# Kernel optimization log

Measured on AMD Instinct MI355X. Metric: run time of the kernel, lower is better.

## Reference

```python
import jax, jax.numpy as jnp
import numpy as np

B, S, D = 64, 512, 256
HG = 128   # graph-RNN hidden
HE = 128   # edge-RNN hidden (must equal HG: graph state seeds edge layer-0 hidden)
M = 64     # edge lookback window / edge-RNN input size


def _rnn_layer(x, Wih, Whh, bih, bhh):
    # tanh-RNN layer, batch_first. x: [B,S,Din] -> [B,S,H]
    def step(h, xt):
        h = jnp.tanh(xt @ Wih.T + bih + h @ Whh.T + bhh)
        return h, h
    h0 = jnp.zeros((x.shape[0], Whh.shape[0]), x.dtype)
    _, ys = jax.lax.scan(step, h0, jnp.swapaxes(x, 0, 1))
    return jnp.swapaxes(ys, 0, 1)


def _forward(x, mask,
             g_Wih0, g_Whh0, g_bih0, g_bhh0,
             g_Wih1, g_Whh1, g_bih1, g_bhh1,
             e_Wih0, e_Whh0, e_bih0, e_bhh0,
             e_Wih1, e_Whh1, e_bih1, e_bhh1,
             cls_W, cls_b):
    # --- node-level (graph) RNN, 2 layers; padded steps zeroed (pad_packed behavior)
    Y = _rnn_layer(x, g_Wih0, g_Whh0, g_bih0, g_bhh0)
    Y = _rnn_layer(Y, g_Wih1, g_Whh1, g_bih1, g_bhh1)
    Y = Y * mask[..., None].astype(Y.dtype)            # [B,S,HG]

    N = B * S
    gs = Y.reshape(N, HG)                              # graph state seeds layer-0 hidden
    node_i = jnp.tile(jnp.arange(S), B)                # position within sequence
    m = jnp.minimum(node_i, M)                         # steps per node = min(i, M)
    A0 = jnp.zeros((N, M), Y.dtype)

    def estep(carry, j):
        A, h0, h1 = carry
        n0 = jnp.tanh(A @ e_Wih0.T + e_bih0 + h0 @ e_Whh0.T + e_bhh0)
        n1 = jnp.tanh(n0 @ e_Wih1.T + e_bih1 + h1 @ e_Whh1.T + e_bhh1)
        s = jax.nn.sigmoid(n1 @ cls_W.T + cls_b)[:, 0]
        A = A.at[:, j].set(jnp.where(j < m, s, jnp.zeros_like(s)))
        return (A, n0, n1), None

    (A, _, _), _ = jax.lax.scan(estep, (A0, gs, jnp.zeros_like(gs)), jnp.arange(M))
    A = A.reshape(B, S, M)

    # --- banded adjacency: row i gets A[i, :min(i,M)] at cols [max(0,i-M), i), then transpose
    i = jnp.arange(S)
    cols = jnp.maximum(0, i - M)[:, None] + jnp.arange(M)[None, :]   # [S,M]
    valid = jnp.arange(M)[None, :] < jnp.minimum(i, M)[:, None]
    cols = jnp.where(valid, cols, S)                                 # OOB -> dropped
    adj = jnp.zeros((B, S, S), Y.dtype).at[:, i[:, None], cols].set(
        A * valid.astype(A.dtype), mode="drop")
    adj = jnp.swapaxes(adj, 1, 2)
    return Y, adj


def setup_inputs() -> dict:
    key = jax.random.key(0)
    ks = jax.random.split(key, 20)
    sc = jnp.float32(0.1)
    p = lambda k, shp: sc * jax.random.normal(k, shp, jnp.float32)
    return {
        "x": jax.random.normal(ks[0], (B, S, D), jnp.float32),
        "mask": jnp.ones((B, S), jnp.int32),
        "g_Wih0": p(ks[1], (HG, D)), "g_Whh0": p(ks[2], (HG, HG)),
        "g_bih0": p(ks[3], (HG,)), "g_bhh0": p(ks[4], (HG,)),
        "g_Wih1": p(ks[5], (HG, HG)), "g_Whh1": p(ks[6], (HG, HG)),
        "g_bih1": p(ks[7], (HG,)), "g_bhh1": p(ks[8], (HG,)),
        "e_Wih0": p(ks[9], (HE, M)), "e_Whh0": p(ks[10], (HE, HE)),
        "e_bih0": p(ks[11], (HE,)), "e_bhh0": p(ks[12], (HE,)),
        "e_Wih1": p(ks[13], (HE, HE)), "e_Whh1": p(ks[14], (HE, HE)),
        "e_bih1": p(ks[15], (HE,)), "e_bhh1": p(ks[16], (HE,)),
        "cls_W": p(ks[17], (1, HE)), "cls_b": p(ks[18], (1,)),
    }


def reference(x, mask,
              g_Wih0, g_Whh0, g_bih0, g_bhh0,
              g_Wih1, g_Whh1, g_bih1, g_bhh1,
              e_Wih0, e_Whh0, e_bih0, e_bhh0,
              e_Wih1, e_Whh1, e_bih1, e_bhh1,
              cls_W, cls_b):
    return _forward(x, mask,
                    g_Wih0, g_Whh0, g_bih0, g_bhh0,
                    g_Wih1, g_Whh1, g_bih1, g_bhh1,
                    e_Wih0, e_Whh0, e_bih0, e_bhh0,
                    e_Wih1, e_Whh1, e_bih1, e_bhh1,
                    cls_W, cls_b)
```

## Files before the change

### kernel.cpp

```cpp
#include <hip/hip_runtime.h>

#define B_ 64
#define S_ 512
#define D_ 256
#define H_ 128
#define M_ 64
#define N_ (B_ * S_)
#define YSZ ((size_t)N_ * H_)
#define ADJSZ ((size_t)B_ * S_ * S_)

typedef __attribute__((ext_vector_type(8))) _Float16 f16x8;
typedef __attribute__((ext_vector_type(2))) _Float16 h2;
typedef __attribute__((ext_vector_type(4))) float f32x4;

#define MFMAH(a, b, c) __builtin_amdgcn_mfma_f32_16x16x32_f16(a, b, c, 0, 0, 0)

#define BARL() asm volatile("s_waitcnt lgkmcnt(0)\n\ts_barrier" ::: "memory")

#if __has_builtin(__builtin_amdgcn_fdot2)
#define FDOT2(a, b, c) __builtin_amdgcn_fdot2((a), (b), (c), false)
#else
__device__ __forceinline__ float FDOT2(h2 a, h2 b, float c) {
  return c + (float)a.x * (float)b.x + (float)a.y * (float)b.y;
}
#endif

#define WFRAGS (8 * 14)
#define WBYTES ((size_t)WFRAGS * 64 * 16)

__device__ __forceinline__ float fast_tanh(float x) {
  float e = __builtin_amdgcn_exp2f(x * 2.8853900817779268f);
  float r = __builtin_amdgcn_rcpf(e + 1.0f);
  return fmaf(-2.0f, r, 1.0f);
}
__device__ __forceinline__ float fast_sigmoid(float x) {
  float e = __builtin_amdgcn_exp2f(x * -1.4426950408889634f);
  return __builtin_amdgcn_rcpf(1.0f + e);
}

__device__ __forceinline__ int sw(int row, int col, int Kc) {
  return row * Kc + ((((col >> 3) ^ (row & 7)) << 3) | (col & 7));
}
__device__ __forceinline__ int swu(int row, int g) {
  return row * 128 + (((g ^ (row & 7)) << 3));
}

__device__ __forceinline__ f16x8 pack8(float4 a, float4 b) {
  f16x8 r;
  r[0] = (_Float16)a.x; r[1] = (_Float16)a.y;
  r[2] = (_Float16)a.z; r[3] = (_Float16)a.w;
  r[4] = (_Float16)b.x; r[5] = (_Float16)b.y;
  r[6] = (_Float16)b.z; r[7] = (_Float16)b.w;
  return r;
}

__global__ __launch_bounds__(256) void k0_prep(
    const float* __restrict__ eWih0, const float* __restrict__ eWhh0,
    const float* __restrict__ eWih1, const float* __restrict__ eWhh1,
    unsigned short* __restrict__ Wf) {
  int t = blockIdx.x * 256 + threadIdx.x;
  if (t >= WFRAGS * 64) return;
  int fid = t >> 6, lane = t & 63;
  int ntg = fid / 14, kc = fid % 14;
  int j = ntg * 16 + (lane & 15);
  int kbase = (kc < 6 ? kc : kc - 6) * 32 + (lane >> 4) * 8;
  unsigned pk[4];
#pragma unroll
  for (int ii = 0; ii < 4; ++ii) {
    unsigned p2 = 0;
#pragma unroll
    for (int s = 0; s < 2; ++s) {
      int k = kbase + ii * 2 + s;
      float wv;
      if (kc < 6)
        wv = (k < 64) ? eWih0[j * 64 + k] : eWhh0[j * 128 + (k - 64)];
      else
        wv = (k < 128) ? eWih1[j * 128 + k] : eWhh1[j * 128 + (k - 128)];
      _Float16 h = (_Float16)wv;
      unsigned short us = *(unsigned short*)&h;
      p2 |= ((unsigned)us) << (16 * s);
    }
    pk[ii] = p2;
  }
  ((uint4*)Wf)[fid * 64 + lane] = make_uint4(pk[0], pk[1], pk[2], pk[3]);
}

__global__ __launch_bounds__(256) void k1_gemm(
    const float* __restrict__ x, const float* __restrict__ W,
    const float* __restrict__ bih, const float* __restrict__ bhh,
    float* __restrict__ P0) {
  __shared__ float Xs[32][132];
  __shared__ float Ws[32][132];
  const int t = threadIdx.x;
  const int ty = t >> 4, tx = t & 15;
  const int n0 = blockIdx.x * 128;
  float acc[8][8];
#pragma unroll
  for (int i = 0; i < 8; ++i)
#pragma unroll
    for (int j = 0; j < 8; ++j) acc[i][j] = 0.f;

  for (int kc = 0; kc < 256; kc += 32) {
    __syncthreads();
#pragma unroll
    for (int l = 0; l < 4; ++l) {
      int idx = t + l * 256;
      int r = idx >> 3, f4 = idx & 7;
      float4 v = *(const float4*)&x[(size_t)(n0 + r) * 256 + kc + f4 * 4];
      Xs[f4 * 4 + 0][r] = v.x; Xs[f4 * 4 + 1][r] = v.y;
      Xs[f4 * 4 + 2][r] = v.z; Xs[f4 * 4 + 3][r] = v.w;
      float4 wv = *(const float4*)&W[(size_t)r * 256 + kc + f4 * 4];
      Ws[f4 * 4 + 0][r] = wv.x; Ws[f4 * 4 + 1][r] = wv.y;
      Ws[f4 * 4 + 2][r] = wv.z; Ws[f4 * 4 + 3][r] = wv.w;
    }
    __syncthreads();
#pragma unroll
    for (int kk = 0; kk < 32; ++kk) {
      float4 xa = *(const float4*)&Xs[kk][ty * 8];
      float4 xb = *(const float4*)&Xs[kk][ty * 8 + 4];
      float4 wa = *(const float4*)&Ws[kk][tx * 8];
      float4 wb = *(const float4*)&Ws[kk][tx * 8 + 4];
      float xr[8] = {xa.x, xa.y, xa.z, xa.w, xb.x, xb.y, xb.z, xb.w};
      float wr[8] = {wa.x, wa.y, wa.z, wa.w, wb.x, wb.y, wb.z, wb.w};
#pragma unroll
      for (int i = 0; i < 8; ++i)
#pragma unroll
        for (int j = 0; j < 8; ++j) acc[i][j] += xr[i] * wr[j];
    }
  }
  float bias[8];
#pragma unroll
  for (int j = 0; j < 8; ++j) bias[j] = bih[tx * 8 + j] + bhh[tx * 8 + j];
#pragma unroll
  for (int i = 0; i < 8; ++i) {
    float4 s0 = make_float4(acc[i][0] + bias[0], acc[i][1] + bias[1],
                            acc[i][2] + bias[2], acc[i][3] + bias[3]);
    float4 s1 = make_float4(acc[i][4] + bias[4], acc[i][5] + bias[5],
                            acc[i][6] + bias[6], acc[i][7] + bias[7]);
    size_t base = (size_t)(n0 + ty * 8 + i) * 128 + tx * 8;
    *(float4*)&P0[base] = s0;
    *(float4*)&P0[base + 4] = s1;
  }
}

#define K2STEP(S, PP)                                                         \
  {                                                                           \
    if (isL0 && (S) < 512) {                                                  \
      const int rd0 = ((S)&1) ^ 1;                                            \
      f32x4 acc[2];                                                           \
      _Pragma("unroll") for (int i = 0; i < 2; ++i)                           \
          acc[i] = __builtin_bit_cast(f32x4, PP[i]);                          \
      _Pragma("unroll") for (int kc = 0; kc < 4; ++kc) {                      \
        f16x8 bf = *(const f16x8*)&h0s[rd0][swu(colB, kc * 4 + q)];           \
        _Pragma("unroll") for (int i = 0; i < 2; ++i)                         \
            acc[i] = MFMAH(WA[i][kc], bf, acc[i]);                            \
      }                                                                       \
      int tn = ((S) + 2 < 512) ? (S) + 2 : 511;                               \
      _Pragma("unroll") for (int i = 0; i < 2; ++i)                           \
          PP[i] = *(const float4*)(p0base[i] + (size_t)tn * 128);             \
      _Pragma("unroll") for (int i = 0; i < 2; ++i) {                         \
        float v0 = fast_tanh(acc[i][0]), v1 = fast_tanh(acc[i][1]);           \
        float v2 = fast_tanh(acc[i][2]), v3 = fast_tanh(acc[i][3]);           \
        int nb = (wl * 2 + i) * 16 + q * 4;                                   \
        int g = nb >> 3;                                                      \
        int idx = colB * 128 + (((g ^ (colB & 7)) << 3) | (nb & 7));          \
        h2 lo = {(_Float16)v0, (_Float16)v1};                                 \
        h2 hi = {(_Float16)v2, (_Float16)v3};                                 \
        uint2 u = {__builtin_bit_cast(unsigned, lo),                          \
                   __builtin_bit_cast(unsigned, hi)};                         \
        *(uint2*)&h0s[(S)&1][idx] = u;                                        \
      }                                                                       \
    } else if (!isL0 && (S) >= 1) {                                           \
      const int t = (S)-1;                                                    \
      const int rb = t & 1;                                                   \
      f32x4 acc[2], accB[2];                                                  \
      _Pragma("unroll") for (int i = 0; i < 2; ++i) {                         \
        acc[i] = b1v[i];                                                      \
        accB[i] = (f32x4){0.f, 0.f, 0.f, 0.f};                                \
      }                                                                       \
      _Pragma("unroll") for (int kc = 0; kc < 4; ++kc) {                      \
        f16x8 bf = *(const f16x8*)&h0s[rb][swu(colB, kc * 4 + q)];            \
        if ((kc & 1) == 0) {                                                  \
          _Pragma("unroll") for (int i = 0; i < 2; ++i)                       \
              acc[i] = MFMAH(WA[i][kc], bf, acc[i]);                          \
        } else {                                                              \
          _Pragma("unroll") for (int i = 0; i < 2; ++i)                       \
              accB[i] = MFMAH(WA[i][kc], bf, accB[i]);                        \
        }                                                                     \
      }                                                                       \
      _Pragma("unroll") for (int kc = 0; kc < 4; ++kc) {                      \
        f16x8 bf = *(const f16x8*)&h1s[rb ^ 1][swu(colB, kc * 4 + q)];        \
        if ((kc & 1) == 0) {                                                  \
          _Pragma("unroll") for (int i = 0; i < 2; ++i)                       \
              acc[i] = MFMAH(WB[i][kc], bf, acc[i]);                          \
        } else {                                                              \
          _Pragma("unroll") for (int i = 0; i < 2; ++i)                       \
              accB[i] = MFMAH(WB[i][kc], bf, accB[i]);                        \
        }                                                                     \
      }                                                                       \
      float m = mk[colB][t];                                                  \
      _Pragma("unroll") for (int i = 0; i < 2; ++i) {                         \
        f32x4 at = acc[i] + accB[i];                                          \
        float v0 = fast_tanh(at[0]), v1 = fast_tanh(at[1]);                   \
        float v2 = fast_tanh(at[2]), v3 = fast_tanh(at[3]);                   \
        int nb = (wl * 2 + i) * 16 + q * 4;                                   \
        int g = nb >> 3;                                                      \
        int idx = colB * 128 + (((g ^ (colB & 7)) << 3) | (nb & 7));          \
        h2 lo = {(_Float16)v0, (_Float16)v1};                                 \
        h2 hi = {(_Float16)v2, (_Float16)v3};                                 \
        uint2 u = {__builtin_bit_cast(unsigned, lo),                          \
                   __builtin_bit_cast(unsigned, hi)};                         \
        *(uint2*)&h1s[rb][idx] = u;                                           \
        float4 yv = {v0 * m, v1 * m, v2 * m, v3 * m};                         \
        *(float4*)&Y[((size_t)(b0 + colB) * 512 + t) * 128 + nb] = yv;        \
      }                                                                       \
    }                                                                         \
    BARL();                                                                   \
  }

__global__ __launch_bounds__(512, 1) void k2_v10(
    const float* __restrict__ P0, const float* __restrict__ Whh0,
    const float* __restrict__ Wih1, const float* __restrict__ Whh1,
    const float* __restrict__ bih1, const float* __restrict__ bhh1,
    const int* __restrict__ mask, float* __restrict__ Y) {
  __shared__ _Float16 h0s[2][16 * 128];
  __shared__ _Float16 h1s[2][16 * 128];
  __shared__ float mk[16][516];
  const int tid = threadIdx.x;
  const int w = tid >> 6, l = tid & 63;
  const int b0 = blockIdx.x * 16;
  const int colB = l & 15;
  const int q = l >> 4;
  const bool isL0 = (w < 4);
  const int wl = isL0 ? w : (w - 4);

  for (int i = tid; i < 16 * 512; i += 512) {
    int bb = i >> 9, t = i & 511;
    mk[bb][t] = (float)mask[(b0 + bb) * 512 + t];
  }
  for (int i = tid; i < 1024; i += 512) {
    ((unsigned*)&h0s[1][0])[i] = 0u;
    ((unsigned*)&h1s[1][0])[i] = 0u;
  }

  f16x8 WA[2][4];
  f16x8 WB[2][4];
  {
    const float* src = isL0 ? Whh0 : Wih1;
#pragma unroll
    for (int i = 0; i < 2; ++i)
#pragma unroll
      for (int kc = 0; kc < 4; ++kc) {
        const float* r =
            src + ((wl * 2 + i) * 16 + colB) * 128 + kc * 32 + q * 8;
        WA[i][kc] = pack8(*(const float4*)r, *(const float4*)(r + 4));
      }
    if (!isL0) {
#pragma unroll
      for (int i = 0; i < 2; ++i)
#pragma unroll
        for (int kc = 0; kc < 4; ++kc) {
          const float* r =
              Whh1 + ((wl * 2 + i) * 16 + colB) * 128 + kc * 32 + q * 8;
          WB[i][kc] = pack8(*(const float4*)r, *(const float4*)(r + 4));
        }
    }
  }
  f32x4 b1v[2];
  const float* p0base[2];
#pragma unroll
  for (int i = 0; i < 2; ++i) {
    int nb = (wl * 2 + i) * 16 + q * 4;
    if (!isL0) {
      b1v[i] = (f32x4){bih1[nb] + bhh1[nb], bih1[nb + 1] + bhh1[nb + 1],
                       bih1[nb + 2] + bhh1[nb + 2], bih1[nb + 3] + bhh1[nb + 3]};
    } else {
      b1v[i] = (f32x4){0.f, 0.f, 0.f, 0.f};
    }
    p0base[i] = P0 + (size_t)(b0 + colB) * 512 * 128 + nb;
  }
  float4 pp0[2], pp1[2];
  if (isL0) {
#pragma unroll
    for (int i = 0; i < 2; ++i) {
      pp0[i] = *(const float4*)(p0base[i]);
      pp1[i] = *(const float4*)(p0base[i] + 128);
    }
  }
  __syncthreads();

  for (int s2 = 0; s2 < 512; s2 += 2) {
    K2STEP(s2, pp0);
    K2STEP(s2 + 1, pp1);
  }
  K2STEP(512, pp0);
}

#define K3_A(g) ((_Float16*)(sm + (g) * 8192))
#define K3_R(g, i) ((_Float16*)(sm + 16384 + ((g) * 3 + (i)) * 16384))
#define K3_PS(g) ((float*)(sm + 114688 + (g) * 1024))
#define LDSTOT 116736

__global__ __launch_bounds__(512, 2) void k3_edge_f16(
    const float* __restrict__ Y, const unsigned short* __restrict__ Wf,
    const float* __restrict__ bih0, const float* __restrict__ bhh0,
    const float* __restrict__ bih1, const float* __restrict__ bhh1,
    const float* __restrict__ clsW, const float* __restrict__ clsb,
    float* __restrict__ adj) {
  extern __shared__ char sm[];
  const int tid = threadIdx.x;
  const int w = tid >> 6, l = tid & 63;
  const int mg = w & 1, ng = w >> 1;
  const int colL = l & 15, q = l >> 4;
  const int node0 = blockIdx.x * 128;

  for (int i = tid; i < 4096; i += 512) ((unsigned*)sm)[i] = 0u;
  for (int i = tid; i < 4096; i += 512) {
    ((unsigned*)K3_R(0, 2))[i] = 0u;
    ((unsigned*)K3_R(1, 2))[i] = 0u;
  }
  for (int i = tid; i < 16384; i += 512) {
    int nn = i >> 7, k = i & 127;
    float v = Y[(size_t)(node0 + nn) * 128 + k];
    K3_R(nn >> 6, 0)[sw(nn & 63, k, 128)] = (_Float16)v;
  }

  f16x8 Wr[2][14];
#pragma unroll
  for (int nt = 0; nt < 2; ++nt)
#pragma unroll
    for (int kc = 0; kc < 14; ++kc)
      Wr[nt][kc] =
          ((const f16x8*)Wf)[(size_t)(((2 * ng + nt) * 14) + kc) * 64 + l];

  f32x4 b0v[2], b1v[2];
  h2 cw2[2][2];
#pragma unroll
  for (int nt = 0; nt < 2; ++nt) {
    int f0 = (2 * ng + nt) * 16 + q * 4;
    b0v[nt] = (f32x4){bih0[f0] + bhh0[f0], bih0[f0 + 1] + bhh0[f0 + 1],
                      bih0[f0 + 2] + bhh0[f0 + 2], bih0[f0 + 3] + bhh0[f0 + 3]};
    b1v[nt] = (f32x4){bih1[f0] + bhh1[f0], bih1[f0 + 1] + bhh1[f0 + 1],
                      bih1[f0 + 2] + bhh1[f0 + 2], bih1[f0 + 3] + bhh1[f0 + 3]};
    cw2[nt][0].x = (_Float16)clsW[f0];
    cw2[nt][0].y = (_Float16)clsW[f0 + 1];
    cw2[nt][1].x = (_Float16)clsW[f0 + 2];
    cw2[nt][1].y = (_Float16)clsW[f0 + 3];
  }
  const float cbias = clsb[0];
  int mval[2];
  mval[0] = min(((node0 + 0) & 511) + l, 64);
  mval[1] = min(((node0 + 64) & 511) + l, 64);

  int woff[2][2];
#pragma unroll
  for (int mt = 0; mt < 2; ++mt)
#pragma unroll
    for (int nt = 0; nt < 2; ++nt) {
      int node = mg * 32 + mt * 16 + colL;
      int f0 = (2 * ng + nt) * 16 + q * 4;
      woff[mt][nt] =
          node * 128 + ((((f0 >> 3) ^ (node & 7)) << 3) | (f0 & 7));
    }

  __syncthreads();

  int ba = 0, bbv = 1, bc = 2;
  for (int step = 0; step < 64; ++step) {
    _Float16* p_n0rd[2] = {K3_R(0, ba), K3_R(1, ba)};
    _Float16* p_n0wr[2] = {K3_R(0, bbv), K3_R(1, bbv)};
    _Float16* p_n1rd[2] = {K3_R(0, bc), K3_R(1, bc)};
    _Float16* p_n1wr[2] = {K3_R(0, ba), K3_R(1, ba)};

    f32x4 acc[2][2][2];
    f32x4 acc2[2][2][2];
#pragma unroll
    for (int g = 0; g < 2; ++g)
#pragma unroll
      for (int mt = 0; mt < 2; ++mt)
#pragma unroll
        for (int nt = 0; nt < 2; ++nt) {
          acc[g][mt][nt] = b0v[nt];
          acc2[g][mt][nt] = b1v[nt];
        }
#pragma unroll
    for (int kc = 0; kc < 4; ++kc) {
      int gk = kc * 4 + q;
      f16x8 bh[2][2];
#pragma unroll
      for (int g = 0; g < 2; ++g)
#pragma unroll
        for (int mt = 0; mt < 2; ++mt) {
          int row = mg * 32 + mt * 16 + colL;
          bh[g][mt] =
              *(const f16x8*)&p_n0rd[g][row * 128 + ((gk ^ (row & 7)) << 3)];
        }
#pragma unroll
      for (int g = 0; g < 2; ++g)
#pragma unroll
        for (int mt = 0; mt < 2; ++mt)
#pragma unroll
          for (int nt = 0; nt < 2; ++nt)
            acc[g][mt][nt] = MFMAH(Wr[nt][2 + kc], bh[g][mt], acc[g][mt][nt]);
    }
#pragma unroll
    for (int kc = 4; kc < 8; ++kc) {
      int gk = (kc & 3) * 4 + q;
      f16x8 bh[2][2];
#pragma unroll
      for (int g = 0; g < 2; ++g)
#pragma unroll
        for (int mt = 0; mt < 2; ++mt) {
          int row = mg * 32 + mt * 16 + colL;
          bh[g][mt] =
              *(const f16x8*)&p_n1rd[g][row * 128 + ((gk ^ (row & 7)) << 3)];
        }
#pragma unroll
      for (int g = 0; g < 2; ++g)
#pragma unroll
        for (int mt = 0; mt < 2; ++mt)
#pragma unroll
          for (int nt = 0; nt < 2; ++nt)
            acc2[g][mt][nt] =
                MFMAH(Wr[nt][6 + kc], bh[g][mt], acc2[g][mt][nt]);
    }
    if (step > 0) {
      {
        int gk = q;
        f16x8 bh[2][2];
#pragma unroll
        for (int g = 0; g < 2; ++g)
#pragma unroll
          for (int mt = 0; mt < 2; ++mt) {
            int row = mg * 32 + mt * 16 + colL;
            bh[g][mt] =
                *(const f16x8*)&K3_A(g)[row * 64 + ((gk ^ (row & 7)) << 3)];
          }
#pragma unroll
        for (int g = 0; g < 2; ++g)
#pragma unroll
          for (int mt = 0; mt < 2; ++mt)
#pragma unroll
            for (int nt = 0; nt < 2; ++nt)
              acc[g][mt][nt] = MFMAH(Wr[nt][0], bh[g][mt], acc[g][mt][nt]);
      }
      if (step > 32) {
        int gk = 4 + q;
        f16x8 bh[2][2];
#pragma unroll
        for (int g = 0; g < 2; ++g)
#pragma unroll
          for (int mt = 0; mt < 2; ++mt) {
            int row = mg * 32 + mt * 16 + colL;
            bh[g][mt] =
                *(const f16x8*)&K3_A(g)[row * 64 + ((gk ^ (row & 7)) << 3)];
          }
#pragma unroll
        for (int g = 0; g < 2; ++g)
#pragma unroll
          for (int mt = 0; mt < 2; ++mt)
#pragma unroll
            for (int nt = 0; nt < 2; ++nt)
              acc[g][mt][nt] = MFMAH(Wr[nt][1], bh[g][mt], acc[g][mt][nt]);
      }
    }
#pragma unroll
    for (int g = 0; g < 2; ++g)
#pragma unroll
      for (int mt = 0; mt < 2; ++mt)
#pragma unroll
        for (int nt = 0; nt < 2; ++nt) {
          float t0 = fast_tanh(acc[g][mt][nt][0]);
          float t1 = fast_tanh(acc[g][mt][nt][1]);
          float t2 = fast_tanh(acc[g][mt][nt][2]);
          float t3 = fast_tanh(acc[g][mt][nt][3]);
          h2 lo = {(_Float16)t0, (_Float16)t1};
          h2 hi = {(_Float16)t2, (_Float16)t3};
          uint2 u = {__builtin_bit_cast(unsigned, lo),
                     __builtin_bit_cast(unsigned, hi)};
          *(uint2*)&p_n0wr[g][woff[mt][nt]] = u;
        }
    __syncthreads();

#pragma unroll
    for (int kc = 0; kc < 4; ++kc) {
      int gk = kc * 4 + q;
      f16x8 bh[2][2];
#pragma unroll
      for (int g = 0; g < 2; ++g)
#pragma unroll
        for (int mt = 0; mt < 2; ++mt) {
          int row = mg * 32 + mt * 16 + colL;
          bh[g][mt] =
              *(const f16x8*)&p_n0wr[g][row * 128 + ((gk ^ (row & 7)) << 3)];
        }
#pragma unroll
      for (int g = 0; g < 2; ++g)
#pragma unroll
        for (int mt = 0; mt < 2; ++mt)
#pragma unroll
          for (int nt = 0; nt < 2; ++nt)
            acc2[g][mt][nt] =
                MFMAH(Wr[nt][6 + kc], bh[g][mt], acc2[g][mt][nt]);
    }
    float paf[2][2];
#pragma unroll
    for (int g = 0; g < 2; ++g)
#pragma unroll
      for (int mt = 0; mt < 2; ++mt) paf[g][mt] = 0.f;
#pragma unroll
    for (int g = 0; g < 2; ++g)
#pragma unroll
      for (int mt = 0; mt < 2; ++mt)
#pragma unroll
        for (int nt = 0; nt < 2; ++nt) {
          float t0 = fast_tanh(acc2[g][mt][nt][0]);
          float t1 = fast_tanh(acc2[g][mt][nt][1]);
          float t2 = fast_tanh(acc2[g][mt][nt][2]);
          float t3 = fast_tanh(acc2[g][mt][nt][3]);
          h2 lo = {(_Float16)t0, (_Float16)t1};
          h2 hi = {(_Float16)t2, (_Float16)t3};
          paf[g][mt] = FDOT2(cw2[nt][0], lo, paf[g][mt]);
          paf[g][mt] = FDOT2(cw2[nt][1], hi, paf[g][mt]);
          uint2 u = {__builtin_bit_cast(unsigned, lo),
                     __builtin_bit_cast(unsigned, hi)};
          *(uint2*)&p_n1wr[g][woff[mt][nt]] = u;
        }
#pragma unroll
    for (int g = 0; g < 2; ++g)
#pragma unroll
      for (int mt = 0; mt < 2; ++mt) {
        float s = paf[g][mt];
        s += __shfl_xor(s, 16);
        s += __shfl_xor(s, 32);
        paf[g][mt] = s;
      }
    if (q == 0) {
#pragma unroll
      for (int g = 0; g < 2; ++g)
#pragma unroll
        for (int mt = 0; mt < 2; ++mt)
          K3_PS(g)[ng * 64 + mg * 32 + mt * 16 + colL] = paf[g][mt];
    }
    __syncthreads();

    {
      float* ps0 = K3_PS(0);
      float* ps1 = K3_PS(1);
      float s0 = cbias + ps0[l] + ps0[64 + l] + ps0[128 + l] + ps0[192 + l];
      float s1 = cbias + ps1[l] + ps1[64 + l] + ps1[128 + l] + ps1[192 + l];
      float sg0 = fast_sigmoid(s0);
      float sg1 = fast_sigmoid(s1);
      int aidx = l * 64 + ((((step >> 3) ^ (l & 7)) << 3) | (step & 7));
      if (step < mval[0]) K3_A(0)[aidx] = (_Float16)sg0;
      if (step < mval[1]) K3_A(1)[aidx] = (_Float16)sg1;
    }
    int tmp = ba; ba = bbv; bbv = bc; bc = tmp;
  }
  __syncthreads();

#pragma unroll
  for (int g = 0; g < 2; ++g) {
    const int qd = l & 15;
    const int rg4 = l >> 4;
    const int node0g = node0 + g * 64;
    const int ii0 = node0g & 511;
    const int badj = node0g >> 9;
    _Float16* Ag = K3_A(g);
    for (int rb = 0; rb < 64; rb += 4) {
      int r = w * 64 + rb + rg4;
      float4 v;
      float* vp = (float*)&v;
#pragma unroll
      for (int c = 0; c < 4; ++c) {
        int n = qd * 4 + c;
        int ii = ii0 + n;
        int base = (ii - 64 > 0) ? ii - 64 : 0;
        int mv = min(ii, 64);
        int k = r - base;
        float val = 0.f;
        if (k >= 0 && k < mv) val = (float)Ag[sw(n, k, 64)];
        vp[c] = val;
      }
      *(float4*)&adj[((size_t)badj * 512 + r) * 512 + ii0 + qd * 4] = v;
    }
  }
}

extern "C" void kernel_launch(void* const* d_in, const int* in_sizes, int n_in,
                              void* d_out, int out_size, void* d_ws,
                              size_t ws_size, hipStream_t stream) {
  const float* x = (const float*)d_in[0];
  const int* mask = (const int*)d_in[1];
  const float* gWih0 = (const float*)d_in[2];
  const float* gWhh0 = (const float*)d_in[3];
  const float* gbih0 = (const float*)d_in[4];
  const float* gbhh0 = (const float*)d_in[5];
  const float* gWih1 = (const float*)d_in[6];
  const float* gWhh1 = (const float*)d_in[7];
  const float* gbih1 = (const float*)d_in[8];
  const float* gbhh1 = (const float*)d_in[9];
  const float* eWih0 = (const float*)d_in[10];
  const float* eWhh0 = (const float*)d_in[11];
  const float* ebih0 = (const float*)d_in[12];
  const float* ebhh0 = (const float*)d_in[13];
  const float* eWih1 = (const float*)d_in[14];
  const float* eWhh1 = (const float*)d_in[15];
  const float* ebih1 = (const float*)d_in[16];
  const float* ebhh1 = (const float*)d_in[17];
  const float* clsW = (const float*)d_in[18];
  const float* clsb = (const float*)d_in[19];
  float* out = (float*)d_out;
  float* Y = out;
  float* adj = out + YSZ;
  float* P0 = adj;

  unsigned short* Wf = (unsigned short*)d_ws;
  hipLaunchKernelGGL(k0_prep, dim3(28), dim3(256), 0, stream, eWih0, eWhh0,
                     eWih1, eWhh1, Wf);
  hipLaunchKernelGGL(k1_gemm, dim3(256), dim3(256), 0, stream, x, gWih0,
                     gbih0, gbhh0, P0);
  hipLaunchKernelGGL(k2_v10, dim3(4), dim3(512), 0, stream, P0, gWhh0, gWih1,
                     gWhh1, gbih1, gbhh1, mask, Y);
  hipFuncSetAttribute(reinterpret_cast<const void*>(k3_edge_f16),
                      hipFuncAttributeMaxDynamicSharedMemorySize, LDSTOT);
  hipLaunchKernelGGL(k3_edge_f16, dim3(256), dim3(512), LDSTOT, stream, Y,
                     Wf, ebih0, ebhh0, ebih1, ebhh1, clsW, clsb, adj);
}
```

Baseline: 601.5 us.

## Rewrite layer-0 input projection GEMM with fp16 MFMA instructions

The input-projection GEMM (x @ Wih0^T + biases) moves from an fp32 scalar-FMA tiled kernel to fp16 MFMA 16x16x32. The whole 128x256 x tile is converted to fp16 and stored in swizzled LDS, and each of 8 waves keeps its 16 weight rows in registers. This cuts the ALU cost of the GEMM in exchange for reduced input precision. The kernel is a small part of the total, since the sequential recurrent kernels probably dominate.

```diff
diff --git a/kernel.cpp b/kernel.cpp
--- a/kernel.cpp
+++ b/kernel.cpp
@@ -85,61 +85,56 @@
   ((uint4*)Wf)[fid * 64 + lane] = make_uint4(pk[0], pk[1], pk[2], pk[3]);
 }
 
-__global__ __launch_bounds__(256) void k1_gemm(
+__global__ __launch_bounds__(512) void k1_mfma(
     const float* __restrict__ x, const float* __restrict__ W,
     const float* __restrict__ bih, const float* __restrict__ bhh,
     float* __restrict__ P0) {
-  __shared__ float Xs[32][132];
-  __shared__ float Ws[32][132];
-  const int t = threadIdx.x;
-  const int ty = t >> 4, tx = t & 15;
+  __shared__ _Float16 Xs[128 * 256];
+  const int tid = threadIdx.x;
+  const int w = tid >> 6, l = tid & 63;
+  const int colL = l & 15, q = l >> 4;
   const int n0 = blockIdx.x * 128;
-  float acc[8][8];
-#pragma unroll
-  for (int i = 0; i < 8; ++i)
-#pragma unroll
-    for (int j = 0; j < 8; ++j) acc[i][j] = 0.f;
-
-  for (int kc = 0; kc < 256; kc += 32) {
-    __syncthreads();
-#pragma unroll
-    for (int l = 0; l < 4; ++l) {
-      int idx = t + l * 256;
-      int r = idx >> 3, f4 = idx & 7;
-      float4 v = *(const float4*)&x[(size_t)(n0 + r) * 256 + kc + f4 * 4];
-      Xs[f4 * 4 + 0][r] = v.x; Xs[f4 * 4 + 1][r] = v.y;
-      Xs[f4 * 4 + 2][r] = v.z; Xs[f4 * 4 + 3][r] = v.w;
-      float4 wv = *(const float4*)&W[(size_t)r * 256 + kc + f4 * 4];
-      Ws[f4 * 4 + 0][r] = wv.x; Ws[f4 * 4 + 1][r] = wv.y;
-      Ws[f4 * 4 + 2][r] = wv.z; Ws[f4 * 4 + 3][r] = wv.w;
-    }
-    __syncthreads();
-#pragma unroll
-    for (int kk = 0; kk < 32; ++kk) {
-      float4 xa = *(const float4*)&Xs[kk][ty * 8];
-      float4 xb = *(const float4*)&Xs[kk][ty * 8 + 4];
-      float4 wa = *(const float4*)&Ws[kk][tx * 8];
-      float4 wb = *(const float4*)&Ws[kk][tx * 8 + 4];
-      float xr[8] = {xa.x, xa.y, xa.z, xa.w, xb.x, xb.y, xb.z, xb.w};
-      float wr[8] = {wa.x, wa.y, wa.z, wa.w, wb.x, wb.y, wb.z, wb.w};
-#pragma unroll
-      for (int i = 0; i < 8; ++i)
-#pragma unroll
-        for (int j = 0; j < 8; ++j) acc[i][j] += xr[i] * wr[j];
-    }
-  }
-  float bias[8];
-#pragma unroll
-  for (int j = 0; j < 8; ++j) bias[j] = bih[tx * 8 + j] + bhh[tx * 8 + j];
-#pragma unroll
-  for (int i = 0; i < 8; ++i) {
-    float4 s0 = make_float4(acc[i][0] + bias[0], acc[i][1] + bias[1],
-                            acc[i][2] + bias[2], acc[i][3] + bias[3]);
-    float4 s1 = make_float4(acc[i][4] + bias[4], acc[i][5] + bias[5],
-                            acc[i][6] + bias[6], acc[i][7] + bias[7]);
-    size_t base = (size_t)(n0 + ty * 8 + i) * 128 + tx * 8;
-    *(float4*)&P0[base] = s0;
-    *(float4*)&P0[base + 4] = s1;
+
+  for (int i = tid; i < 8192; i += 512) {
+    int nn = i >> 6, f4 = (i & 63) * 4;
+    float4 v = *(const float4*)&x[(size_t)(n0 + nn) * 256 + f4];
+    h2 lo = {(_Float16)v.x, (_Float16)v.y};
+    h2 hi = {(_Float16)v.z, (_Float16)v.w};
+    uint2 u = {__builtin_bit_cast(unsigned, lo),
+               __builtin_bit_cast(unsigned, hi)};
+    *(uint2*)&Xs[sw(nn, f4, 256)] = u;
+  }
+  f16x8 Wr[8];
+#pragma unroll
+  for (int kc = 0; kc < 8; ++kc) {
+    const float* r = W + (w * 16 + colL) * 256 + kc * 32 + q * 8;
+    Wr[kc] = pack8(*(const float4*)r, *(const float4*)(r + 4));
+  }
+  f32x4 bv;
+  {
+    int f0 = w * 16 + q * 4;
+    bv = (f32x4){bih[f0] + bhh[f0], bih[f0 + 1] + bhh[f0 + 1],
+                 bih[f0 + 2] + bhh[f0 + 2], bih[f0 + 3] + bhh[f0 + 3]};
+  }
+  __syncthreads();
+
+  f32x4 acc[8];
+#pragma unroll
+  for (int mt = 0; mt < 8; ++mt) acc[mt] = bv;
+#pragma unroll
+  for (int kc = 0; kc < 8; ++kc) {
+    int gk = kc * 4 + q;
+#pragma unroll
+    for (int mt = 0; mt < 8; ++mt) {
+      int row = mt * 16 + colL;
+      f16x8 bf = *(const f16x8*)&Xs[row * 256 + ((gk ^ (row & 7)) << 3)];
+      acc[mt] = MFMAH(Wr[kc], bf, acc[mt]);
+    }
+  }
+#pragma unroll
+  for (int mt = 0; mt < 8; ++mt) {
+    float4 s = {acc[mt][0], acc[mt][1], acc[mt][2], acc[mt][3]};
+    *(float4*)&P0[(size_t)(n0 + mt * 16 + colL) * 128 + w * 16 + q * 4] = s;
   }
 }
 
@@ -618,7 +613,7 @@
   unsigned short* Wf = (unsigned short*)d_ws;
   hipLaunchKernelGGL(k0_prep, dim3(28), dim3(256), 0, stream, eWih0, eWhh0,
                      eWih1, eWhh1, Wf);
-  hipLaunchKernelGGL(k1_gemm, dim3(256), dim3(256), 0, stream, x, gWih0,
+  hipLaunchKernelGGL(k1_mfma, dim3(256), dim3(512), 0, stream, x, gWih0,
                      gbih0, gbhh0, P0);
   hipLaunchKernelGGL(k2_v10, dim3(4), dim3(512), 0, stream, P0, gWhh0, gWih1,
                      gWhh1, gbih1, gbhh1, mask, Y);
```

Result: faster. 576.2 us (-4.2%).
